# Kernel optimization log

Hardware: AMD Instinct MI355X
Metric: run time of the kernel (lower is better)

The kernel has to match this reference:

```python
import jax, jax.numpy as jnp
from jax import lax
import numpy as np

B, L, D, H, SH = 4, 1024, 512, 8, 256
MLP_H = 4 * D
GAMMA, BETA = 0.1, 1.0
SIG_A, SIG_B = 1.0, 0.5
BIG = 1e9


def setup_inputs() -> dict:
    key = jax.random.key(0)
    ks = jax.random.split(key, 8)

    def lin(k, fin, fout):
        return jax.random.normal(k, (fin, fout), jnp.float32) * (1.0 / np.sqrt(fin))

    inp = {}
    inp["x"] = jax.random.normal(ks[0], (B, L, D), jnp.float32)
    inp["ln1_g"] = jnp.ones((D,), jnp.float32)
    inp["ln1_b"] = jnp.zeros((D,), jnp.float32)
    inp["ln2_g"] = jnp.ones((D,), jnp.float32)
    inp["ln2_b"] = jnp.zeros((D,), jnp.float32)
    inp["qkv_w"] = lin(ks[1], D, 3 * D)
    inp["qkv_b"] = jnp.zeros((3 * D,), jnp.float32)
    inp["proj_w"] = lin(ks[2], D, D)
    inp["proj_b"] = jnp.zeros((D,), jnp.float32)
    inp["fc1_w"] = lin(ks[3], D, MLP_H)
    inp["fc1_b"] = jnp.zeros((MLP_H,), jnp.float32)
    inp["fc2_w"] = lin(ks[4], MLP_H, D)
    inp["fc2_b"] = jnp.zeros((D,), jnp.float32)
    # 4 SigmaNets (norm1, attn, norm2, mlp) stacked on leading axis
    inp["sig_w1"] = jax.random.normal(ks[5], (4, D, SH), jnp.float32) * (1.0 / np.sqrt(D))
    inp["sig_b1"] = jnp.zeros((4, SH), jnp.float32)
    inp["sig_w2"] = jax.random.normal(ks[6], (4, SH, D), jnp.float32) * (1.0 / np.sqrt(SH))
    inp["sig_b2"] = jnp.zeros((4, D), jnp.float32)
    return inp


def layernorm(x, g, b, eps=1e-5):
    m = x.mean(-1, keepdims=True)
    v = ((x - m) ** 2).mean(-1, keepdims=True)
    return (x - m) / jnp.sqrt(v + eps) * g + b


def sigmanet(x, w1, b1, w2, b2):
    # (B,L,D) -> (B,L,1), sigma = a*sigmoid(mean(fc2(relu(fc1(x))))) + b
    h = jax.nn.relu(x @ w1 + b1)
    o = h @ w2 + b2
    m = o.mean(-1, keepdims=True)
    return SIG_A * jax.nn.sigmoid(m) + SIG_B


def attention(x, qkv_w, qkv_b, proj_w, proj_b):
    b_, l_, d_ = x.shape
    hd = d_ // H
    qkv = (x @ qkv_w + qkv_b).reshape(b_, l_, 3, H, hd)
    q, k, v = qkv[:, :, 0], qkv[:, :, 1], qkv[:, :, 2]  # (B,L,H,hd)
    scores = jnp.einsum("bqhd,bkhd->bhqk", q, k) * (hd ** -0.5)
    attn = jax.nn.softmax(scores, axis=-1)
    out = jnp.einsum("bhqk,bkhd->bqhd", attn, v).reshape(b_, l_, d_)
    return out @ proj_w + proj_b


def mlp(x, fc1_w, fc1_b, fc2_w, fc2_b):
    return jax.nn.gelu(x @ fc1_w + fc1_b, approximate=False) @ fc2_w + fc2_b


def soft_dtw(C, gamma):
    # soft-min DP over (B, N, N) cost matrix via anti-diagonal scan
    b_, n_, m_ = C.shape
    i_arr = jnp.arange(n_)

    def step(carry, k):
        d2, d1 = carry  # diagonals k-2, k-1; entry i holds R[i, (k-?)-i]
        j = k - i_arr
        valid = (j >= 0) & (j < m_)
        jc = jnp.clip(j, 0, m_ - 1)
        Cd = jnp.where(valid[None, :], C[:, i_arr, jc], BIG)
        pad = jnp.full((b_, 1), BIG, C.dtype)
        a = jnp.concatenate([pad, d2[:, :-1]], axis=1)  # R[i-1, j-1]
        a = a.at[:, 0].set(jnp.where(k == 0, 0.0, a[:, 0]))  # virtual R[-1,-1]=0
        bdiag = jnp.concatenate([pad, d1[:, :-1]], axis=1)  # R[i-1, j]
        c = d1  # R[i, j-1]
        smin = -gamma * jax.nn.logsumexp(-jnp.stack([a, bdiag, c], 0) / gamma, axis=0)
        new = jnp.where(valid[None, :], Cd + smin, BIG)
        return (d1, new), None

    init = (jnp.full((b_, n_), BIG, C.dtype), jnp.full((b_, n_), BIG, C.dtype))
    (_, last), _ = lax.scan(step, init, jnp.arange(n_ + m_ - 1))
    return last[:, n_ - 1]  # R[N-1, M-1]


def udtw(x, y, sx, sy):
    # pairwise squared distances without (B,L,L,D) intermediate
    x2 = jnp.sum(x * x, -1)  # (B,L)
    y2 = jnp.sum(y * y, -1)
    Dm = x2[:, :, None] + y2[:, None, :] - 2.0 * jnp.einsum("bnd,bmd->bnm", x, y)
    Dm = jnp.maximum(Dm, 0.0)
    Sig = sx ** 2 + jnp.swapaxes(sy, 1, 2) ** 2  # (B,L,L) sigma_i^2 + sigma_j^2
    d = soft_dtw(Dm / Sig, GAMMA)               # uncertainty-weighted distance path
    s = soft_dtw(BETA * jnp.log(Sig), GAMMA)    # sigma regularization path
    return d, s


def reference(x, ln1_g, ln1_b, ln2_g, ln2_b, qkv_w, qkv_b, proj_w, proj_b,
              fc1_w, fc1_b, fc2_w, fc2_b, sig_w1, sig_b1, sig_w2, sig_b2):
    orig = x
    attn_out = attention(layernorm(x, ln1_g, ln1_b), qkv_w, qkv_b, proj_w, proj_b)
    sigma_x = sigmanet(orig, sig_w1[0], sig_b1[0], sig_w2[0], sig_b2[0])
    sigma_attn = sigmanet(attn_out, sig_w1[1], sig_b1[1], sig_w2[1], sig_b2[1])
    d_a, s_a = udtw(orig, attn_out, sigma_x, sigma_attn)
    x = x + attn_out * sigma_attn  # merge_mode == 'mul'
    mlp_out = mlp(layernorm(x, ln2_g, ln2_b), fc1_w, fc1_b, fc2_w, fc2_b)
    sigma_x2 = sigmanet(orig, sig_w1[2], sig_b1[2], sig_w2[2], sig_b2[2])
    sigma_mlp = sigmanet(mlp_out, sig_w1[3], sig_b1[3], sig_w2[3], sig_b2[3])
    d_m, s_m = udtw(orig, mlp_out, sigma_x2, sigma_mlp)
    l_ = x.shape[1]
    aux_loss = (d_a.mean() + s_a.mean() + d_m.mean() + s_m.mean()) / (l_ * l_)
    x = x + mlp_out * sigma_mlp
    return x, aux_loss
```

## Files before the change

### kernel.cpp

```cpp
#include <hip/hip_runtime.h>
#include <math.h>

typedef unsigned short ushort;
typedef __attribute__((ext_vector_type(8))) short short8;
typedef __attribute__((ext_vector_type(4))) short short4v;
typedef __attribute__((ext_vector_type(4))) float f32x4;

#define DEVI static __device__ __forceinline__

constexpr int Bq = 4, Lq = 1024, Dq = 512, Hq = 8, SHq = 256;
constexpr int Mrows = Bq * Lq;
constexpr float BIGF = 1e9f;
constexpr int PSTR = 1048576 + 16;

DEVI float bf2f(ushort u) { union { unsigned u; float f; } v; v.u = ((unsigned)u) << 16; return v.f; }
DEVI float bf2f(short s) { return bf2f((ushort)s); }
DEVI ushort f2bf(float f) {
  union { float f; unsigned u; } v; v.f = f;
  unsigned r = v.u + 0x7fffu + ((v.u >> 16) & 1u);
  return (ushort)(r >> 16);
}
DEVI float wave_sum(float x) { for (int o = 1; o < 64; o <<= 1) x += __shfl_xor(x, o, 64); return x; }
DEVI float readin(const void* p, long i, int isf32) {
  return isf32 ? ((const float*)p)[i] : bf2f(((const ushort*)p)[i]);
}

__global__ void detect_kern(const unsigned* __restrict__ g, int* __restrict__ flag) {
  if (threadIdx.x == 0) flag[0] = (g[0] == 0x3F800000u) ? 1 : 0;
}

__global__ __launch_bounds__(256) void convx_kern(const void* __restrict__ src, ushort* __restrict__ dst,
                                                  long n, const int* __restrict__ flag) {
  const int f = *flag;
  for (long i = blockIdx.x * 256L + threadIdx.x; i < n; i += (long)gridDim.x * 256)
    dst[i] = f ? f2bf(((const float*)src)[i]) : ((const ushort*)src)[i];
}

__global__ __launch_bounds__(256) void conv9_kern(const void* p0, const void* p1, const void* p2,
                                                  const void* p3, const void* p4, const void* p5,
                                                  const void* p6, const void* p7, const void* p8,
                                                  ushort* __restrict__ dst, const int* __restrict__ flag) {
  const int off[10] = {0, 512, 1024, 1536, 2048, 3584, 4096, 6144, 6656, 7680};
  const void* ps[9] = {p0, p1, p2, p3, p4, p5, p6, p7, p8};
  const int b = blockIdx.x;
  const void* s = ps[b];
  const int n = off[b + 1] - off[b];
  const int f = *flag;
  for (int i = threadIdx.x; i < n; i += 256)
    dst[off[b] + i] = f ? f2bf(((const float*)s)[i]) : ((const ushort*)s)[i];
}

__global__ __launch_bounds__(256) void transpose_bf(const void* __restrict__ src,
                                                    ushort* __restrict__ dst, int R, int C,
                                                    const int* __restrict__ flag) {
  __shared__ ushort t[64][65];
  const int f = *flag;
  const int tx = threadIdx.x & 63, tg = threadIdx.x >> 6;
  const long base = (long)blockIdx.z * R * C;
  const int r0 = blockIdx.y * 64, c0 = blockIdx.x * 64;
#pragma unroll
  for (int i = 0; i < 16; ++i) {
    int y = tg * 16 + i;
    float v = readin(src, base + (long)(r0 + y) * C + c0 + tx, f);
    t[y][tx] = f2bf(v);
  }
  __syncthreads();
#pragma unroll
  for (int i = 0; i < 16; ++i) {
    int y = tg * 16 + i;
    dst[base + (long)(c0 + y) * R + r0 + tx] = t[tx][y];
  }
}

__global__ void w2bar_kern(const void* __restrict__ w2, float* __restrict__ w2bar,
                           const int* __restrict__ flag) {
  const int k = blockIdx.x, s = blockIdx.y, lane = threadIdx.x;
  const int f = *flag;
  float t = 0.f;
#pragma unroll
  for (int i = 0; i < 8; ++i) t += readin(w2, ((long)s * SHq + k) * Dq + lane * 8 + i, f);
  t = wave_sum(t);
  if (lane == 0) w2bar[s * SHq + k] = t * (1.f / Dq);
}
__global__ void b2bar_kern(const void* __restrict__ b2, float* __restrict__ b2bar,
                           const int* __restrict__ flag) {
  const int s = blockIdx.x, lane = threadIdx.x;
  const int f = *flag;
  float t = 0.f;
#pragma unroll
  for (int i = 0; i < 8; ++i) t += readin(b2, (long)s * Dq + lane * 8 + i, f);
  t = wave_sum(t);
  if (lane == 0) b2bar[s] = t * (1.f / Dq);
}

__global__ __launch_bounds__(256) void ln_kern(const ushort* __restrict__ x, const ushort* __restrict__ g,
                                               const ushort* __restrict__ b, ushort* __restrict__ out) {
  const int row = blockIdx.x * 4 + (threadIdx.x >> 6);
  const int lane = threadIdx.x & 63;
  short8 v = *(const short8*)(x + (long)row * Dq + lane * 8);
  float f[8]; float s = 0.f, s2 = 0.f;
#pragma unroll
  for (int i = 0; i < 8; ++i) { f[i] = bf2f(v[i]); s += f[i]; s2 += f[i] * f[i]; }
  s = wave_sum(s); s2 = wave_sum(s2);
  float mean = s * (1.f / Dq);
  float var = s2 * (1.f / Dq) - mean * mean;
  float rstd = rsqrtf(var + 1e-5f);
  short8 gv = *(const short8*)(g + lane * 8);
  short8 bv = *(const short8*)(b + lane * 8);
  short8 o;
#pragma unroll
  for (int i = 0; i < 8; ++i) o[i] = (short)f2bf((f[i] - mean) * rstd * bf2f(gv[i]) + bf2f(bv[i]));
  *(short8*)(out + (long)row * Dq + lane * 8) = o;
}

template<int EPI>
__global__ __launch_bounds__(256) void gemm_kern(
    const ushort* __restrict__ A, int lda, long sA,
    const ushort* __restrict__ Bt, int ldb, long sB,
    const ushort* __restrict__ bias,
    void* __restrict__ Cout, int ldc, long sC, int K,
    const float* __restrict__ vx2, const float* __restrict__ vy2,
    const float* __restrict__ vsx, const float* __restrict__ vsy) {
  constexpr int LDT = 40;
  __shared__ alignas(16) short As[128 * LDT];
  __shared__ alignas(16) short Bs[128 * LDT];
  const int tid = threadIdx.x, lane = tid & 63, wid = tid >> 6;
  const int wr = wid >> 1, wc = wid & 1;
  const int m0 = blockIdx.y * 128, n0 = blockIdx.x * 128;
  const int bz = blockIdx.z;
  const ushort* Ab = A + (long)bz * sA;
  const ushort* Bb = Bt + (long)bz * sB;
  const int sr = tid >> 2, sc = (tid & 3) * 8;
  const int lr = lane & 15, lk = (lane >> 4) * 8;
  f32x4 acc[4][4];
#pragma unroll
  for (int i = 0; i < 4; ++i)
#pragma unroll
    for (int j = 0; j < 4; ++j) acc[i][j] = f32x4{0.f, 0.f, 0.f, 0.f};

  for (int k0 = 0; k0 < K; k0 += 32) {
    short8 a0 = *(const short8*)(Ab + (long)(m0 + sr) * lda + k0 + sc);
    short8 a1 = *(const short8*)(Ab + (long)(m0 + sr + 64) * lda + k0 + sc);
    short8 b0 = *(const short8*)(Bb + (long)(n0 + sr) * ldb + k0 + sc);
    short8 b1 = *(const short8*)(Bb + (long)(n0 + sr + 64) * ldb + k0 + sc);
    __syncthreads();
    *(short8*)&As[sr * LDT + sc] = a0;
    *(short8*)&As[(sr + 64) * LDT + sc] = a1;
    *(short8*)&Bs[sr * LDT + sc] = b0;
    *(short8*)&Bs[(sr + 64) * LDT + sc] = b1;
    __syncthreads();
    short8 af[4], bg[4];
#pragma unroll
    for (int m = 0; m < 4; ++m) af[m] = *(const short8*)&As[(wr * 64 + m * 16 + lr) * LDT + lk];
#pragma unroll
    for (int n = 0; n < 4; ++n) bg[n] = *(const short8*)&Bs[(wc * 64 + n * 16 + lr) * LDT + lk];
#pragma unroll
    for (int m = 0; m < 4; ++m)
#pragma unroll
      for (int n = 0; n < 4; ++n)
        acc[m][n] = __builtin_amdgcn_mfma_f32_16x16x32_bf16(af[m], bg[n], acc[m][n], 0, 0, 0);
  }
  const int lq = (lane >> 4) * 4;
#pragma unroll
  for (int n = 0; n < 4; ++n) {
    const int col = n0 + wc * 64 + n * 16 + lr;
    float bia = 0.f, y2v = 0.f, syv = 0.f;
    if (EPI <= 2) { if (bias) bia = bf2f(bias[col]); }
    if (EPI == 3) { y2v = vy2[(long)bz * Lq + col]; float t = vsy[(long)bz * Lq + col]; syv = t * t; }
#pragma unroll
    for (int m = 0; m < 4; ++m) {
      f32x4 v = acc[m][n];
      if (EPI <= 2) {
#pragma unroll
        for (int q = 0; q < 4; ++q) {
          const int row = m0 + wr * 64 + m * 16 + lq + q;
          float c = v[q] + bia;
          if (EPI == 1) c = fmaxf(c, 0.f);
          if (EPI == 2) c = 0.5f * c * (1.f + erff(c * 0.70710678118654752f));
          ((ushort*)Cout)[(long)bz * sC + (long)row * ldc + col] = f2bf(c);
        }
      } else {
        const int row0 = m0 + wr * 64 + m * 16 + lq;
        f32x4 o;
#pragma unroll
        for (int q = 0; q < 4; ++q) {
          float x2v = vx2[(long)bz * Lq + row0 + q];
          float sxv = vsx[(long)bz * Lq + row0 + q];
          float dm = fmaxf(x2v + y2v - 2.f * v[q], 0.f);
          o[q] = dm / (sxv * sxv + syv);
        }
        *(f32x4*)((float*)Cout + (long)bz * sC + (long)col * 1024 + row0) = o;
      }
    }
  }
}

__global__ __launch_bounds__(256) void attn_kern(const ushort* __restrict__ qkv, ushort* __restrict__ octx) {
  const int qt = blockIdx.x, h = blockIdx.y, b = blockIdx.z;
  const int tid = threadIdx.x, lane = tid & 63, wid = tid >> 6;
  const int lr = lane & 15, lkg = lane >> 4;
  __shared__ alignas(16) short Ks[64 * 72];
  __shared__ alignas(16) short Vt[64 * 72];
  __shared__ alignas(16) short Ps[64 * 72];
  const long qrow0 = (long)b * Lq + qt * 64;
  short8 qf[2];
  {
    const ushort* qp = qkv + (qrow0 + wid * 16 + lr) * 1536 + h * 64;
    qf[0] = *(const short8*)(qp + lkg * 8);
    qf[1] = *(const short8*)(qp + 32 + lkg * 8);
  }
  f32x4 accO[4];
#pragma unroll
  for (int n = 0; n < 4; ++n) accO[n] = f32x4{0.f, 0.f, 0.f, 0.f};
  float mrun[4], lrun[4];
#pragma unroll
  for (int q = 0; q < 4; ++q) { mrun[q] = -1e30f; lrun[q] = 0.f; }

  for (int t = 0; t < 16; ++t) {
    __syncthreads();
#pragma unroll
    for (int i = 0; i < 2; ++i) {
      const int row = (tid >> 3) + i * 32;
      const int c8 = (tid & 7) * 8;
      const long gr = ((long)b * Lq + t * 64 + row) * 1536 + h * 64;
      short8 kv = *(const short8*)(qkv + gr + 512 + c8);
      *(short8*)&Ks[row * 72 + c8] = kv;
      short8 vv = *(const short8*)(qkv + gr + 1024 + c8);
#pragma unroll
      for (int j = 0; j < 8; ++j) Vt[(c8 + j) * 72 + row] = vv[j];
    }
    __syncthreads();
    f32x4 sf[4];
#pragma unroll
    for (int n = 0; n < 4; ++n) {
      sf[n] = f32x4{0.f, 0.f, 0.f, 0.f};
#pragma unroll
      for (int ks = 0; ks < 2; ++ks) {
        short8 bk = *(const short8*)&Ks[(n * 16 + lr) * 72 + ks * 32 + lkg * 8];
        sf[n] = __builtin_amdgcn_mfma_f32_16x16x32_bf16(qf[ks], bk, sf[n], 0, 0, 0);
      }
    }
#pragma unroll
    for (int n = 0; n < 4; ++n)
#pragma unroll
      for (int q = 0; q < 4; ++q) sf[n][q] *= 0.125f;
    float scl[4];
#pragma unroll
    for (int q = 0; q < 4; ++q) {
      float mx = fmaxf(fmaxf(sf[0][q], sf[1][q]), fmaxf(sf[2][q], sf[3][q]));
#pragma unroll
      for (int o = 1; o < 16; o <<= 1) mx = fmaxf(mx, __shfl_xor(mx, o, 64));
      float mnew = fmaxf(mrun[q], mx);
      scl[q] = __expf(mrun[q] - mnew);
      mrun[q] = mnew;
      float rs = 0.f;
#pragma unroll
      for (int n = 0; n < 4; ++n) { float pp = __expf(sf[n][q] - mnew); sf[n][q] = pp; rs += pp; }
#pragma unroll
      for (int o = 1; o < 16; o <<= 1) rs += __shfl_xor(rs, o, 64);
      lrun[q] = lrun[q] * scl[q] + rs;
    }
#pragma unroll
    for (int n = 0; n < 4; ++n)
#pragma unroll
      for (int q = 0; q < 4; ++q) accO[n][q] *= scl[q];
#pragma unroll
    for (int n = 0; n < 4; ++n)
#pragma unroll
      for (int q = 0; q < 4; ++q)
        Ps[(wid * 16 + lkg * 4 + q) * 72 + n * 16 + lr] = (short)f2bf(sf[n][q]);
    short8 pa[2];
    pa[0] = *(const short8*)&Ps[(wid * 16 + lr) * 72 + lkg * 8];
    pa[1] = *(const short8*)&Ps[(wid * 16 + lr) * 72 + 32 + lkg * 8];
#pragma unroll
    for (int n = 0; n < 4; ++n)
#pragma unroll
      for (int ks = 0; ks < 2; ++ks) {
        short8 bv = *(const short8*)&Vt[(n * 16 + lr) * 72 + ks * 32 + lkg * 8];
        accO[n] = __builtin_amdgcn_mfma_f32_16x16x32_bf16(pa[ks], bv, accO[n], 0, 0, 0);
      }
  }
#pragma unroll
  for (int n = 0; n < 4; ++n) {
    const int col = h * 64 + n * 16 + lr;
#pragma unroll
    for (int q = 0; q < 4; ++q) {
      const long row = qrow0 + wid * 16 + lkg * 4 + q;
      octx[row * 512 + col] = f2bf(accO[n][q] / fmaxf(lrun[q], 1e-30f));
    }
  }
}

__global__ __launch_bounds__(256) void rownorm2_kern(const ushort* __restrict__ x, float* __restrict__ out) {
  const int row = blockIdx.x * 4 + (threadIdx.x >> 6), lane = threadIdx.x & 63;
  short8 v = *(const short8*)(x + (long)row * Dq + lane * 8);
  float s = 0.f;
#pragma unroll
  for (int i = 0; i < 8; ++i) { float f = bf2f(v[i]); s += f * f; }
  s = wave_sum(s);
  if (lane == 0) out[row] = s;
}

__global__ __launch_bounds__(256) void sigma_reduce_kern(const ushort* __restrict__ h, const float* __restrict__ w2bar,
                                                         const float* __restrict__ b2bar, int set,
                                                         float* __restrict__ sigma) {
  const int row = blockIdx.x * 4 + (threadIdx.x >> 6), lane = threadIdx.x & 63;
  short4v hv = *(const short4v*)(h + (long)row * SHq + lane * 4);
  float s = 0.f;
#pragma unroll
  for (int i = 0; i < 4; ++i) s += bf2f(hv[i]) * w2bar[lane * 4 + i];
  s = wave_sum(s);
  if (lane == 0) {
    float m = s + b2bar[set];
    sigma[(long)set * Mrows + row] = 1.f / (1.f + __expf(-m)) + 0.5f;
  }
}

__global__ __launch_bounds__(256) void fuse1_kern(const ushort* __restrict__ x, const ushort* __restrict__ attn,
                                                  const float* __restrict__ sig, const ushort* __restrict__ g,
                                                  const ushort* __restrict__ bb, void* __restrict__ x1out,
                                                  ushort* __restrict__ xn2, const int* __restrict__ flag) {
  const int row = blockIdx.x * 4 + (threadIdx.x >> 6), lane = threadIdx.x & 63;
  const int isf32 = *flag;
  const float sg = sig[row];
  short8 xv = *(const short8*)(x + (long)row * Dq + lane * 8);
  short8 av = *(const short8*)(attn + (long)row * Dq + lane * 8);
  float f[8]; float s = 0.f, s2 = 0.f;
#pragma unroll
  for (int i = 0; i < 8; ++i) {
    f[i] = bf2f(xv[i]) + bf2f(av[i]) * sg;
    s += f[i]; s2 += f[i] * f[i];
  }
  if (isf32) {
    float* o32 = (float*)x1out + (long)row * Dq + lane * 8;
    *(f32x4*)o32 = f32x4{f[0], f[1], f[2], f[3]};
    *(f32x4*)(o32 + 4) = f32x4{f[4], f[5], f[6], f[7]};
  } else {
    short8 xo;
#pragma unroll
    for (int i = 0; i < 8; ++i) xo[i] = (short)f2bf(f[i]);
    *(short8*)((ushort*)x1out + (long)row * Dq + lane * 8) = xo;
  }
  s = wave_sum(s); s2 = wave_sum(s2);
  float mean = s * (1.f / Dq);
  float var = s2 * (1.f / Dq) - mean * mean;
  float rstd = rsqrtf(var + 1e-5f);
  short8 gv = *(const short8*)(g + lane * 8);
  short8 bv = *(const short8*)(bb + lane * 8);
  short8 o;
#pragma unroll
  for (int i = 0; i < 8; ++i) o[i] = (short)f2bf((f[i] - mean) * rstd * bf2f(gv[i]) + bf2f(bv[i]));
  *(short8*)(xn2 + (long)row * Dq + lane * 8) = o;
}

__global__ __launch_bounds__(256) void fuse2_kern(const ushort* __restrict__ mlp,
                                                  const float* __restrict__ sig, void* __restrict__ out,
                                                  const int* __restrict__ flag) {
  const int row = blockIdx.x * 4 + (threadIdx.x >> 6), lane = threadIdx.x & 63;
  const int isf32 = *flag;
  const float sg = sig[row];
  short8 mv = *(const short8*)(mlp + (long)row * Dq + lane * 8);
  if (isf32) {
    float* o32 = (float*)out + (long)row * Dq + lane * 8;
    f32x4 a = *(const f32x4*)o32;
    f32x4 b = *(const f32x4*)(o32 + 4);
#pragma unroll
    for (int i = 0; i < 4; ++i) a[i] += bf2f(mv[i]) * sg;
#pragma unroll
    for (int i = 0; i < 4; ++i) b[i] += bf2f(mv[4 + i]) * sg;
    *(f32x4*)o32 = a;
    *(f32x4*)(o32 + 4) = b;
  } else {
    ushort* o16 = (ushort*)out + (long)row * Dq + lane * 8;
    short8 xv = *(const short8*)o16;
    short8 o;
#pragma unroll
    for (int i = 0; i < 8; ++i) o[i] = (short)f2bf(bf2f(xv[i]) + bf2f(mv[i]) * sg);
    *(short8*)o16 = o;
  }
}

__global__ __launch_bounds__(128, 1) void dtw_kern(const float* __restrict__ Cta, const float* __restrict__ Ctm,
                                                   const float* __restrict__ sigma, float* __restrict__ res) {
  const int sid = blockIdx.x >> 2, b = blockIdx.x & 3;
  const int tid = threadIdx.x, lane = tid & 63, wid = tid >> 6;
  const bool isS = (sid & 1);
  __shared__ alignas(16) float smemf[20480];
  constexpr float LN2 = 0.69314718055994531f;

  float cur[16];
#pragma unroll
  for (int r = 0; r < 16; ++r) cur[r] = BIGF;
  float topNew = BIGF;
  float topOld = (lane == 0) ? 0.f : BIGF;

  if (!isS) {
    const float* Ct = ((sid == 0) ? Cta : Ctm) + (long)b * PSTR;

#define PRODUCE(S0)                                                            \
    {                                                                          \
      f32x4 L[8][4];                                                           \
      _Pragma("unroll")                                                        \
      for (int j = 0; j < 8; ++j) {                                            \
        int col = (S0) + j - lane;                                             \
        col = col < 0 ? 0 : (col > 1023 ? 1023 : col);                         \
        const float* gp = Ct + (long)col * 1024 + lane * 16;                   \
        _Pragma("unroll")                                                      \
        for (int q = 0; q < 4; ++q) L[j][q] = *(const f32x4*)(gp + q * 4);     \
      }                                                                        \
      __builtin_amdgcn_sched_barrier(0);                                       \
      _Pragma("unroll")                                                        \
      for (int j = 0; j < 8; ++j) {                                            \
        float* lp = &smemf[(((S0) + j) & 15) * 1280 + lane * 20];              \
        _Pragma("unroll")                                                      \
        for (int q = 0; q < 4; ++q) *(f32x4*)(lp + q * 4) = L[j][q];           \
      }                                                                        \
    }

#define LOADQ(RR, S)                                                           \
    {                                                                          \
      const float* lp = &smemf[((S) & 15) * 1280 + lane * 20];                 \
      _Pragma("unroll")                                                        \
      for (int q = 0; q < 4; ++q) RR[q] = *(const f32x4*)(lp + q * 4);         \
    }

#define DCHAIN(S, RR, CHK)                                                     \
    {                                                                          \
      const int c = (S) - lane;                                                \
      const bool valid = (unsigned)c < 1024u;                                  \
      float above = topNew, diag = topOld;                                     \
      _Pragma("unroll")                                                        \
      for (int i = 0; i < 16; ++i) {                                           \
        float tmp = cur[i];                                                    \
        float v = RR[i >> 2][i & 3] + fminf(fminf(above, tmp), diag);          \
        cur[i] = (CHK) ? (valid ? v : tmp) : v;                                \
        diag = tmp; above = v;                                                 \
      }                                                                        \
      topOld = topNew;                                                         \
      float bshf = __shfl_up(cur[15], 1, 64);                                  \
      topNew = (lane == 0) ? BIGF : bshf;                                      \
    }

#define DPHASE(S0, CHK)                                                        \
    {                                                                          \
      f32x4 r0[4], r1[4], r2[4], r3[4], r4[4], r5[4], r6[4], r7[4];            \
      LOADQ(r0, (S0) + 0) LOADQ(r1, (S0) + 1) LOADQ(r2, (S0) + 2)              \
      LOADQ(r3, (S0) + 3) LOADQ(r4, (S0) + 4) LOADQ(r5, (S0) + 5)              \
      LOADQ(r6, (S0) + 6) LOADQ(r7, (S0) + 7)                                  \
      DCHAIN((S0) + 0, r0, CHK) DCHAIN((S0) + 1, r1, CHK)                      \
      DCHAIN((S0) + 2, r2, CHK) DCHAIN((S0) + 3, r3, CHK)                      \
      DCHAIN((S0) + 4, r4, CHK) DCHAIN((S0) + 5, r5, CHK)                      \
      DCHAIN((S0) + 6, r6, CHK) DCHAIN((S0) + 7, r7, CHK)                      \
    }

    if (wid == 1) PRODUCE(0)
    __syncthreads();
#pragma clang loop unroll(disable)
    for (int p = 0; p < 8; ++p) {
      if (wid == 1) { PRODUCE(8 * p + 8) } else { DPHASE(8 * p, 1) }
      __syncthreads();
    }
#pragma clang loop unroll(disable)
    for (int p = 8; p < 128; ++p) {
      if (wid == 1) { PRODUCE(8 * p + 8) } else { DPHASE(8 * p, 0) }
      __syncthreads();
    }
#pragma clang loop unroll(disable)
    for (int p = 128; p < 136; ++p) {
      if (wid == 1) { if (p < 135) PRODUCE(8 * p + 8) } else { DPHASE(8 * p, 1) }
      __syncthreads();
    }
#undef PRODUCE
#undef LOADQ
#undef DCHAIN
#undef DPHASE
    if (wid == 0 && lane == 63) res[blockIdx.x] = cur[15];
  } else {
    const int sxset = (sid == 1) ? 0 : 2;
    const float* sxv = sigma + (long)sxset * Mrows + b * Lq;
    const float* syv = sigma + (long)(sxset + 1) * Mrows + b * Lq;
    for (int i = tid; i < Lq; i += 128) { float v = syv[i]; smemf[i] = v * v; }
    __syncthreads();
    if (wid == 1) return;
    float sx2[16];
#pragma unroll
    for (int r = 0; r < 16; ++r) { float t = sxv[16 * lane + r]; sx2[r] = t * t; }
    int c0i = 0 - lane; c0i = c0i < 0 ? 0 : c0i;
    float sy2_cur = smemf[c0i];

#define SSTEP(S, CHK)                                                          \
    {                                                                          \
      int cn = (S) + 1 - lane; cn = cn < 0 ? 0 : (cn > 1023 ? 1023 : cn);      \
      float sy2_nxt = smemf[cn];                                               \
      const int c = (S) - lane;                                                \
      const bool valid = (unsigned)c < 1024u;                                  \
      float above = topNew, diag = topOld;                                     \
      _Pragma("unroll")                                                        \
      for (int i = 0; i < 16; ++i) {                                           \
        float tmp = cur[i];                                                    \
        float cv = LN2 * __builtin_amdgcn_logf(sx2[i] + sy2_cur);              \
        float v = cv + fminf(fminf(above, tmp), diag);                         \
        cur[i] = (CHK) ? (valid ? v : tmp) : v;                                \
        diag = tmp; above = v;                                                 \
      }                                                                        \
      sy2_cur = sy2_nxt;                                                       \
      topOld = topNew;                                                         \
      float bshf = __shfl_up(cur[15], 1, 64);                                  \
      topNew = (lane == 0) ? BIGF : bshf;                                      \
    }

#pragma clang loop unroll(disable)
    for (int s = 0; s < 63; ++s) SSTEP(s, 1)
#pragma clang loop unroll(disable)
    for (int s = 63; s < 1024; ++s) SSTEP(s, 0)
#pragma clang loop unroll(disable)
    for (int s = 1024; s < 1088; ++s) SSTEP(s, 1)
#undef SSTEP
    if (lane == 63) res[blockIdx.x] = cur[15];
  }
}

__global__ void aux_kern(const float* __restrict__ res, void* __restrict__ out,
                         const int* __restrict__ flag) {
  if (threadIdx.x == 0) {
    float s = 0.f;
    for (int i = 0; i < 16; ++i) s += res[i];
    float v = s * (0.25f / (1024.f * 1024.f));
    if (*flag) ((float*)out)[(size_t)Mrows * 512] = v;
    else       ((ushort*)out)[(size_t)Mrows * 512] = f2bf(v);
  }
}

extern "C" void kernel_launch(void* const* d_in, const int* in_sizes, int n_in,
                              void* d_out, int out_size, void* d_ws, size_t ws_size,
                              hipStream_t stream) {
  const void* x_raw   = d_in[0];
  const void* ln1_g   = d_in[1];
  const void* ln1_b   = d_in[2];
  const void* ln2_g   = d_in[3];
  const void* ln2_b   = d_in[4];
  const void* qkv_w   = d_in[5];
  const void* qkv_b   = d_in[6];
  const void* proj_w  = d_in[7];
  const void* proj_b  = d_in[8];
  const void* fc1_w   = d_in[9];
  const void* fc1_b   = d_in[10];
  const void* fc2_w   = d_in[11];
  const void* fc2_b   = d_in[12];
  const void* sig_w1  = d_in[13];
  const void* sig_b1  = d_in[14];
  const void* sig_w2  = d_in[15];
  const void* sig_b2  = d_in[16];

  char* p = (char*)d_ws;
  auto alloc = [&](size_t n) { char* r = p; p += (n + 255) & ~(size_t)255; return r; };
  const size_t REGION = (size_t)4 * PSTR * 4;
  int*    flag    = (int*)alloc(256);
  ushort* csmall  = (ushort*)alloc(7680 * 2);
  ushort* x_bf    = (ushort*)alloc((size_t)Mrows * 512 * 2);
  ushort* wt_qkv  = (ushort*)alloc((size_t)1536 * 512 * 2);
  ushort* wt_proj = (ushort*)alloc((size_t)512 * 512 * 2);
  ushort* wt_fc1  = (ushort*)alloc((size_t)2048 * 512 * 2);
  ushort* wt_fc2  = (ushort*)alloc((size_t)512 * 2048 * 2);
  ushort* wt_sig1 = (ushort*)alloc((size_t)4 * 256 * 512 * 2);
  float*  w2bar   = (float*)alloc(4 * 256 * 4);
  float*  b2bar   = (float*)alloc(4 * 4);
  ushort* xnorm   = (ushort*)alloc((size_t)Mrows * 512 * 2);
  char* region1 = alloc(REGION);
  ushort* qkvb     = (ushort*)region1;
  ushort* attn_ctx = (ushort*)(region1 + (size_t)Mrows * 1536 * 2);
  float*  Cta      = (float*)region1;
  ushort* abuf   = (ushort*)alloc((size_t)Mrows * 512 * 2);
  ushort* hsig   = (ushort*)alloc((size_t)Mrows * 256 * 2);
  float*  sigma  = (float*)alloc((size_t)4 * Mrows * 4);
  float*  x2n    = (float*)alloc(Mrows * 4);
  float*  y2a    = (float*)alloc(Mrows * 4);
  float*  y2m    = (float*)alloc(Mrows * 4);
  char* region2 = alloc(REGION);
  ushort* h1  = (ushort*)region2;
  float*  Ctm = (float*)region2;
  float*  dres = (float*)alloc(64 * 4);

  const ushort* c_ln1g = csmall + 0;
  const ushort* c_ln1b = csmall + 512;
  const ushort* c_ln2g = csmall + 1024;
  const ushort* c_ln2b = csmall + 1536;
  const ushort* c_qkvb = csmall + 2048;
  const ushort* c_projb = csmall + 3584;
  const ushort* c_fc1b = csmall + 4096;
  const ushort* c_fc2b = csmall + 6144;
  const ushort* c_sigb1 = csmall + 6656;

  detect_kern<<<1, 64, 0, stream>>>((const unsigned*)ln1_g, flag);
  conv9_kern<<<9, 256, 0, stream>>>(ln1_g, ln1_b, ln2_g, ln2_b, qkv_b, proj_b, fc1_b, fc2_b, sig_b1,
                                    csmall, flag);
  convx_kern<<<2048, 256, 0, stream>>>(x_raw, x_bf, (long)Mrows * 512, flag);

  transpose_bf<<<dim3(24, 8, 1), 256, 0, stream>>>(qkv_w, wt_qkv, 512, 1536, flag);
  transpose_bf<<<dim3(8, 8, 1), 256, 0, stream>>>(proj_w, wt_proj, 512, 512, flag);
  transpose_bf<<<dim3(32, 8, 1), 256, 0, stream>>>(fc1_w, wt_fc1, 512, 2048, flag);
  transpose_bf<<<dim3(8, 32, 1), 256, 0, stream>>>(fc2_w, wt_fc2, 2048, 512, flag);
  transpose_bf<<<dim3(4, 8, 4), 256, 0, stream>>>(sig_w1, wt_sig1, 512, 256, flag);
  w2bar_kern<<<dim3(256, 4), 64, 0, stream>>>(sig_w2, w2bar, flag);
  b2bar_kern<<<4, 64, 0, stream>>>(sig_b2, b2bar, flag);

  ln_kern<<<Mrows / 4, 256, 0, stream>>>(x_bf, c_ln1g, c_ln1b, xnorm);
  gemm_kern<0><<<dim3(12, 32, 1), 256, 0, stream>>>(xnorm, 512, 0, wt_qkv, 512, 0, c_qkvb,
                                                    qkvb, 1536, 0, 512, nullptr, nullptr, nullptr, nullptr);
  attn_kern<<<dim3(16, 8, 4), 256, 0, stream>>>(qkvb, attn_ctx);
  gemm_kern<0><<<dim3(4, 32, 1), 256, 0, stream>>>(attn_ctx, 512, 0, wt_proj, 512, 0, c_projb,
                                                   abuf, 512, 0, 512, nullptr, nullptr, nullptr, nullptr);
  gemm_kern<1><<<dim3(2, 32, 1), 256, 0, stream>>>(x_bf, 512, 0, wt_sig1, 512, 0, c_sigb1,
                                                   hsig, 256, 0, 512, nullptr, nullptr, nullptr, nullptr);
  sigma_reduce_kern<<<Mrows / 4, 256, 0, stream>>>(hsig, w2bar, b2bar, 0, sigma);
  gemm_kern<1><<<dim3(2, 32, 1), 256, 0, stream>>>(abuf, 512, 0, wt_sig1 + 1 * 256 * 512, 512, 0, c_sigb1 + 256,
                                                   hsig, 256, 0, 512, nullptr, nullptr, nullptr, nullptr);
  sigma_reduce_kern<<<Mrows / 4, 256, 0, stream>>>(hsig, w2bar + 256, b2bar, 1, sigma);
  rownorm2_kern<<<Mrows / 4, 256, 0, stream>>>(x_bf, x2n);
  rownorm2_kern<<<Mrows / 4, 256, 0, stream>>>(abuf, y2a);
  gemm_kern<3><<<dim3(8, 8, 4), 256, 0, stream>>>(x_bf, 512, (long)1024 * 512, abuf, 512, (long)1024 * 512, nullptr,
                                                  Cta, 1024, (long)PSTR, 512, x2n, y2a, sigma, sigma + Mrows);
  fuse1_kern<<<Mrows / 4, 256, 0, stream>>>(x_bf, abuf, sigma + Mrows, c_ln2g, c_ln2b, d_out, xnorm, flag);
  gemm_kern<2><<<dim3(16, 32, 1), 256, 0, stream>>>(xnorm, 512, 0, wt_fc1, 512, 0, c_fc1b,
                                                    h1, 2048, 0, 512, nullptr, nullptr, nullptr, nullptr);
  gemm_kern<0><<<dim3(4, 32, 1), 256, 0, stream>>>(h1, 2048, 0, wt_fc2, 2048, 0, c_fc2b,
                                                   abuf, 512, 0, 2048, nullptr, nullptr, nullptr, nullptr);
  gemm_kern<1><<<dim3(2, 32, 1), 256, 0, stream>>>(x_bf, 512, 0, wt_sig1 + 2 * 256 * 512, 512, 0, c_sigb1 + 512,
                                                   hsig, 256, 0, 512, nullptr, nullptr, nullptr, nullptr);
  sigma_reduce_kern<<<Mrows / 4, 256, 0, stream>>>(hsig, w2bar + 512, b2bar, 2, sigma);
  gemm_kern<1><<<dim3(2, 32, 1), 256, 0, stream>>>(abuf, 512, 0, wt_sig1 + 3 * 256 * 512, 512, 0, c_sigb1 + 768,
                                                   hsig, 256, 0, 512, nullptr, nullptr, nullptr, nullptr);
  sigma_reduce_kern<<<Mrows / 4, 256, 0, stream>>>(hsig, w2bar + 768, b2bar, 3, sigma);
  rownorm2_kern<<<Mrows / 4, 256, 0, stream>>>(abuf, y2m);
  gemm_kern<3><<<dim3(8, 8, 4), 256, 0, stream>>>(x_bf, 512, (long)1024 * 512, abuf, 512, (long)1024 * 512, nullptr,
                                                  Ctm, 1024, (long)PSTR, 512, x2n, y2m,
                                                  sigma + 2 * Mrows, sigma + 3 * Mrows);
  fuse2_kern<<<Mrows / 4, 256, 0, stream>>>(abuf, sigma + 3 * Mrows, d_out, flag);
  dtw_kern<<<16, 128, 0, stream>>>(Cta, Ctm, sigma, dres);
  aux_kern<<<1, 64, 0, stream>>>(dres, d_out, flag);
}
```

Before: 581.6 us.

## Process two DTW columns per wavefront step to halve cross-lane shuffle latency chain

Reworks the wavefront skew in the DTW kernels so each lane advances two columns per step instead of one. Lanes are now offset by two columns, which cuts the number of serialized shuffle-and-propagate steps from about 1088 to about 576 for both the distance and sigma paths. The shared-memory staging buffer is reorganised to hold column pairs, with 8 slots of 2560 floats. In exchange, each step carries a longer dependent chain of 32 min/add operations and more register pressure.

```diff
diff --git a/kernel.cpp b/kernel.cpp
--- a/kernel.cpp
+++ b/kernel.cpp
@@ -391,89 +391,96 @@
   float cur[16];
 #pragma unroll
   for (int r = 0; r < 16; ++r) cur[r] = BIGF;
-  float topNew = BIGF;
-  float topOld = (lane == 0) ? 0.f : BIGF;
+  float A = BIGF;
+  float B = BIGF;
+  float D = (lane == 0) ? 0.f : BIGF;
 
   if (!isS) {
     const float* Ct = ((sid == 0) ? Cta : Ctm) + (long)b * PSTR;
 
-#define PRODUCE(S0)                                                            \
+#define PRODUCE2(S0)                                                           \
     {                                                                          \
-      f32x4 L[8][4];                                                           \
+      f32x4 L[4][8];                                                           \
       _Pragma("unroll")                                                        \
-      for (int j = 0; j < 8; ++j) {                                            \
-        int col = (S0) + j - lane;                                             \
-        col = col < 0 ? 0 : (col > 1023 ? 1023 : col);                         \
-        const float* gp = Ct + (long)col * 1024 + lane * 16;                   \
+      for (int j = 0; j < 4; ++j) {                                            \
+        const int ss = (S0) + j;                                               \
+        int cA = 2 * ss - 2 * lane;                                            \
+        int cB = cA + 1;                                                       \
+        cA = cA < 0 ? 0 : (cA > 1023 ? 1023 : cA);                             \
+        cB = cB < 0 ? 0 : (cB > 1023 ? 1023 : cB);                             \
+        const float* gA = Ct + (long)cA * 1024 + lane * 16;                    \
+        const float* gB = Ct + (long)cB * 1024 + lane * 16;                    \
         _Pragma("unroll")                                                      \
-        for (int q = 0; q < 4; ++q) L[j][q] = *(const f32x4*)(gp + q * 4);     \
+        for (int q = 0; q < 4; ++q) { L[j][q] = *(const f32x4*)(gA + q * 4);   \
+                                      L[j][4 + q] = *(const f32x4*)(gB + q * 4); } \
       }                                                                        \
       __builtin_amdgcn_sched_barrier(0);                                       \
       _Pragma("unroll")                                                        \
-      for (int j = 0; j < 8; ++j) {                                            \
-        float* lp = &smemf[(((S0) + j) & 15) * 1280 + lane * 20];              \
+      for (int j = 0; j < 4; ++j) {                                            \
+        float* lp = &smemf[(((S0) + j) & 7) * 2560 + lane * 40];               \
         _Pragma("unroll")                                                      \
-        for (int q = 0; q < 4; ++q) *(f32x4*)(lp + q * 4) = L[j][q];           \
+        for (int q = 0; q < 4; ++q) { *(f32x4*)(lp + q * 4) = L[j][q];         \
+                                      *(f32x4*)(lp + 16 + q * 4) = L[j][4 + q]; } \
       }                                                                        \
     }
 
-#define LOADQ(RR, S)                                                           \
+#define DSTEP2(S, CHK)                                                         \
     {                                                                          \
-      const float* lp = &smemf[((S) & 15) * 1280 + lane * 20];                 \
+      const float* lp = &smemf[((S) & 7) * 2560 + lane * 40];                  \
+      f32x4 ra[4], rb[4];                                                      \
       _Pragma("unroll")                                                        \
-      for (int q = 0; q < 4; ++q) RR[q] = *(const f32x4*)(lp + q * 4);         \
-    }
-
-#define DCHAIN(S, RR, CHK)                                                     \
-    {                                                                          \
-      const int c = (S) - lane;                                                \
-      const bool valid = (unsigned)c < 1024u;                                  \
-      float above = topNew, diag = topOld;                                     \
+      for (int q = 0; q < 4; ++q) { ra[q] = *(const f32x4*)(lp + q * 4);       \
+                                    rb[q] = *(const f32x4*)(lp + 16 + q * 4); } \
+      const int c1 = 2 * (S) - 2 * lane;                                       \
+      const bool v1 = (unsigned)c1 < 1024u;                                    \
+      const bool v2 = (unsigned)(c1 + 1) < 1024u;                              \
+      float above = A, diag = D;                                               \
       _Pragma("unroll")                                                        \
       for (int i = 0; i < 16; ++i) {                                           \
         float tmp = cur[i];                                                    \
-        float v = RR[i >> 2][i & 3] + fminf(fminf(above, tmp), diag);          \
-        cur[i] = (CHK) ? (valid ? v : tmp) : v;                                \
+        float v = ra[i >> 2][i & 3] + fminf(fminf(above, tmp), diag);          \
+        cur[i] = (CHK) ? (v1 ? v : tmp) : v;                                   \
         diag = tmp; above = v;                                                 \
       }                                                                        \
-      topOld = topNew;                                                         \
-      float bshf = __shfl_up(cur[15], 1, 64);                                  \
-      topNew = (lane == 0) ? BIGF : bshf;                                      \
-    }
-
-#define DPHASE(S0, CHK)                                                        \
-    {                                                                          \
-      f32x4 r0[4], r1[4], r2[4], r3[4], r4[4], r5[4], r6[4], r7[4];            \
-      LOADQ(r0, (S0) + 0) LOADQ(r1, (S0) + 1) LOADQ(r2, (S0) + 2)              \
-      LOADQ(r3, (S0) + 3) LOADQ(r4, (S0) + 4) LOADQ(r5, (S0) + 5)              \
-      LOADQ(r6, (S0) + 6) LOADQ(r7, (S0) + 7)                                  \
-      DCHAIN((S0) + 0, r0, CHK) DCHAIN((S0) + 1, r1, CHK)                      \
-      DCHAIN((S0) + 2, r2, CHK) DCHAIN((S0) + 3, r3, CHK)                      \
-      DCHAIN((S0) + 4, r4, CHK) DCHAIN((S0) + 5, r5, CHK)                      \
-      DCHAIN((S0) + 6, r6, CHK) DCHAIN((S0) + 7, r7, CHK)                      \
-    }
-
-    if (wid == 1) PRODUCE(0)
+      float bot1 = cur[15];                                                    \
+      above = B; diag = A;                                                     \
+      _Pragma("unroll")                                                        \
+      for (int i = 0; i < 16; ++i) {                                           \
+        float tmp = cur[i];                                                    \
+        float v = rb[i >> 2][i & 3] + fminf(fminf(above, tmp), diag);          \
+        cur[i] = (CHK) ? (v2 ? v : tmp) : v;                                   \
+        diag = tmp; above = v;                                                 \
+      }                                                                        \
+      float bot2 = cur[15];                                                    \
+      D = B;                                                                   \
+      float sA = __shfl_up(bot1, 1, 64);                                       \
+      float sB = __shfl_up(bot2, 1, 64);                                       \
+      A = (lane == 0) ? BIGF : sA;                                             \
+      B = (lane == 0) ? BIGF : sB;                                             \
+    }
+
+    if (wid == 1) PRODUCE2(0)
     __syncthreads();
 #pragma clang loop unroll(disable)
-    for (int p = 0; p < 8; ++p) {
-      if (wid == 1) { PRODUCE(8 * p + 8) } else { DPHASE(8 * p, 1) }
+    for (int p = 0; p < 16; ++p) {
+      if (wid == 1) { PRODUCE2(4 * p + 4) }
+      else { const int s0 = 4 * p; DSTEP2(s0, 1) DSTEP2(s0 + 1, 1) DSTEP2(s0 + 2, 1) DSTEP2(s0 + 3, 1) }
       __syncthreads();
     }
 #pragma clang loop unroll(disable)
-    for (int p = 8; p < 128; ++p) {
-      if (wid == 1) { PRODUCE(8 * p + 8) } else { DPHASE(8 * p, 0) }
+    for (int p = 16; p < 128; ++p) {
+      if (wid == 1) { PRODUCE2(4 * p + 4) }
+      else { const int s0 = 4 * p; DSTEP2(s0, 0) DSTEP2(s0 + 1, 0) DSTEP2(s0 + 2, 0) DSTEP2(s0 + 3, 0) }
       __syncthreads();
     }
 #pragma clang loop unroll(disable)
-    for (int p = 128; p < 136; ++p) {
-      if (wid == 1) { if (p < 135) PRODUCE(8 * p + 8) } else { DPHASE(8 * p, 1) }
+    for (int p = 128; p < 144; ++p) {
+      if (wid == 1) { if (p < 143) PRODUCE2(4 * p + 4) }
+      else { const int s0 = 4 * p; DSTEP2(s0, 1) DSTEP2(s0 + 1, 1) DSTEP2(s0 + 2, 1) DSTEP2(s0 + 3, 1) }
       __syncthreads();
     }
-#undef PRODUCE
-#undef LOADQ
-#undef DCHAIN
-#undef DPHASE
+#undef PRODUCE2
+#undef DSTEP2
     if (wid == 0 && lane == 63) res[blockIdx.x] = cur[15];
   } else {
     const int sxset = (sid == 1) ? 0 : 2;
@@ -485,37 +492,52 @@
     float sx2[16];
 #pragma unroll
     for (int r = 0; r < 16; ++r) { float t = sxv[16 * lane + r]; sx2[r] = t * t; }
-    int c0i = 0 - lane; c0i = c0i < 0 ? 0 : c0i;
-    float sy2_cur = smemf[c0i];
-
-#define SSTEP(S, CHK)                                                          \
+    int ia = -2 * lane; ia = ia < 0 ? 0 : ia;
+    int ib = 1 - 2 * lane; ib = ib < 0 ? 0 : ib;
+    float syA = smemf[ia], syB = smemf[ib];
+
+#define SSTEP2(S, CHK)                                                         \
     {                                                                          \
-      int cn = (S) + 1 - lane; cn = cn < 0 ? 0 : (cn > 1023 ? 1023 : cn);      \
-      float sy2_nxt = smemf[cn];                                               \
-      const int c = (S) - lane;                                                \
-      const bool valid = (unsigned)c < 1024u;                                  \
-      float above = topNew, diag = topOld;                                     \
+      int na = 2 * ((S) + 1) - 2 * lane; na = na < 0 ? 0 : (na > 1023 ? 1023 : na); \
+      int nb = na + 1; nb = nb > 1023 ? 1023 : nb;                             \
+      float syA_n = smemf[na], syB_n = smemf[nb];                              \
+      const int c1 = 2 * (S) - 2 * lane;                                       \
+      const bool v1 = (unsigned)c1 < 1024u;                                    \
+      const bool v2 = (unsigned)(c1 + 1) < 1024u;                              \
+      float above = A, diag = D;                                               \
       _Pragma("unroll")                                                        \
       for (int i = 0; i < 16; ++i) {                                           \
         float tmp = cur[i];                                                    \
-        float cv = LN2 * __builtin_amdgcn_logf(sx2[i] + sy2_cur);              \
+        float cv = LN2 * __builtin_amdgcn_logf(sx2[i] + syA);                  \
         float v = cv + fminf(fminf(above, tmp), diag);                         \
-        cur[i] = (CHK) ? (valid ? v : tmp) : v;                                \
+        cur[i] = (CHK) ? (v1 ? v : tmp) : v;                                   \
         diag = tmp; above = v;                                                 \
       }                                                                        \
-      sy2_cur = sy2_nxt;                                                       \
-      topOld = topNew;                                                         \
-      float bshf = __shfl_up(cur[15], 1, 64);                                  \
-      topNew = (lane == 0) ? BIGF : bshf;                                      \
+      float bot1 = cur[15];                                                    \
+      above = B; diag = A;                                                     \
+      _Pragma("unroll")                                                        \
+      for (int i = 0; i < 16; ++i) {                                           \
+        float tmp = cur[i];                                                    \
+        float cv = LN2 * __builtin_amdgcn_logf(sx2[i] + syB);                  \
+        float v = cv + fminf(fminf(above, tmp), diag);                         \
+        cur[i] = (CHK) ? (v2 ? v : tmp) : v;                                   \
+        diag = tmp; above = v;                                                 \
+      }                                                                        \
+      float bot2 = cur[15];                                                    \
+      D = B; syA = syA_n; syB = syB_n;                                         \
+      float sA = __shfl_up(bot1, 1, 64);                                       \
+      float sB = __shfl_up(bot2, 1, 64);                                       \
+      A = (lane == 0) ? BIGF : sA;                                             \
+      B = (lane == 0) ? BIGF : sB;                                             \
     }
 
 #pragma clang loop unroll(disable)
-    for (int s = 0; s < 63; ++s) SSTEP(s, 1)
+    for (int s = 0; s < 63; ++s) SSTEP2(s, 1)
 #pragma clang loop unroll(disable)
-    for (int s = 63; s < 1024; ++s) SSTEP(s, 0)
+    for (int s = 63; s < 512; ++s) SSTEP2(s, 0)
 #pragma clang loop unroll(disable)
-    for (int s = 1024; s < 1088; ++s) SSTEP(s, 1)
-#undef SSTEP
+    for (int s = 512; s < 576; ++s) SSTEP2(s, 1)
+#undef SSTEP2
     if (lane == 63) res[blockIdx.x] = cur[15];
   }
 }
```

Measured after the change: 549.0 us. 1.06x faster.
